# Kernel tuning notes

Hardware: AMD Instinct MI355X
Metric: run time of the kernel (lower is better)

## Reference

```python
import jax, jax.numpy as jnp
import numpy as np

H, HKV, HD = 16, 16, 64  # num_heads, num_kv_heads, head_dim

def rotate_half(x):
    x1, x2 = jnp.split(x, 2, axis=-1)
    return jnp.concatenate((-x2, x1), axis=-1)

def setup_inputs() -> dict:
    key = jax.random.key(0)
    ks = jax.random.split(key, 4)
    B, L, D = 4, 2048, 1024
    hidden_states = jax.random.normal(ks[0], (B, L, D), jnp.float32)
    # RoPE tables [L, head_dim]
    inv_freq = 1.0 / (10000.0 ** (jnp.arange(0, HD, 2, dtype=jnp.float32) / HD))
    freqs = jnp.outer(jnp.arange(L, dtype=jnp.float32), inv_freq)
    emb = jnp.concatenate((freqs, freqs), axis=-1)
    cos, sin = jnp.cos(emb), jnp.sin(emb)
    active_mask = jax.random.randint(ks[1], (B, L), 0, 2).astype(bool)
    Wqkv = jax.random.normal(ks[2], ((H + 2 * HKV) * HD, D), jnp.float32) / np.sqrt(D)
    Wo = jax.random.normal(ks[3], (D, H * HD), jnp.float32) / np.sqrt(H * HD)
    return {"hidden_states": hidden_states, "cos": cos, "sin": sin,
            "active_mask": active_mask, "Wqkv": Wqkv, "Wo": Wo}

def reference(hidden_states, cos, sin, active_mask, Wqkv, Wo):
    B, L, D = hidden_states.shape
    qkv = (hidden_states @ Wqkv.T).reshape(B, L, H + 2 * HKV, HD)
    q = qkv[:, :, :H]
    k = qkv[:, :, H:H + HKV]
    v = qkv[:, :, H + HKV:]
    c = cos[:, None, :]  # [L,1,HD] broadcasts over B and heads
    s = sin[:, None, :]
    q = q * c + rotate_half(q) * s
    k = k * c + rotate_half(k) * s
    # sparse queries: only active positions emit queries
    q = q * active_mask[:, :, None, None].astype(q.dtype)
    scale = 1.0 / np.sqrt(HD)
    scores = jnp.einsum('bqhd,bkhd->bhqk', q, k) * scale  # [B,H,L,L]
    attn = jax.nn.softmax(scores, axis=-1)
    out = jnp.einsum('bhqk,bkhd->bqhd', attn, v).reshape(B, L, H * HD)
    out = out @ Wo.T
    return out * active_mask[:, :, None].astype(out.dtype)
```

## Files before the change

### kernel.cpp

```cpp
#include <hip/hip_runtime.h>
#include <cstdint>

typedef _Float16 f16;
typedef __attribute__((ext_vector_type(2))) __fp16 fp16v2;
typedef __attribute__((ext_vector_type(4))) _Float16 f16x4;
typedef __attribute__((ext_vector_type(8))) _Float16 f16x8;
typedef __attribute__((ext_vector_type(4))) float f32x4;
typedef __attribute__((ext_vector_type(16))) float f32x16;

#if __has_builtin(__builtin_amdgcn_exp2f)
#define EXP2F(x) __builtin_amdgcn_exp2f(x)
#else
#define EXP2F(x) exp2f(x)
#endif

#if __has_builtin(__builtin_amdgcn_fdot2)
#define FDOT2(a, b, c) __builtin_amdgcn_fdot2((a), (b), (c), false)
#else
#define FDOT2(a, b, c) ((c) + (float)(a)[0] * (float)(b)[0] + (float)(a)[1] * (float)(b)[1])
#endif

#define GLOAD_LDS16(gp, lp) \
  __builtin_amdgcn_global_load_lds((const __attribute__((address_space(1))) void*)(gp), \
                                   (__attribute__((address_space(3))) void*)(lp), 16, 0, 0)

__global__ __launch_bounds__(256) void cvt_all(const float4* __restrict__ h, f16x4* __restrict__ h16,
                                               const float4* __restrict__ wq, f16x4* __restrict__ wq16,
                                               const float4* __restrict__ wo, f16x4* __restrict__ wo16,
                                               const float* __restrict__ cosb, const float* __restrict__ sinb,
                                               float2* __restrict__ cst) {
  int i = blockIdx.x * 256 + threadIdx.x;
  if (i >= 3145728) {
    const int i2 = i - 3145728;
    const int d = i2 >> 11, l = i2 & 2047;
    cst[i2] = make_float2(cosb[l * 64 + d], sinb[l * 64 + d]);
    return;
  }
  const float4* src;
  f16x4* dst;
  if (i < 2097152) { src = h + i; dst = h16 + i; }
  else if (i < 2883584) { src = wq + (i - 2097152); dst = wq16 + (i - 2097152); }
  else { src = wo + (i - 2883584); dst = wo16 + (i - 2883584); }
  float4 v = *src;
  f16x4 o;
  o.x = (f16)v.x; o.y = (f16)v.y; o.z = (f16)v.z; o.w = (f16)v.w;
  *dst = o;
}

template<int EPI, int N, int K>
__global__ __launch_bounds__(512) void gemm_bt2(
    const f16* __restrict__ A, const f16* __restrict__ Bm,
    f16* __restrict__ Qf, f16* __restrict__ Kf, f16* __restrict__ Vf,
    float* __restrict__ Cout, const int* __restrict__ mask,
    const float2* __restrict__ cst) {
  constexpr int NT = N / 128;
  constexpr int NKT = K / 64;
  const int tid = threadIdx.x;
  const int lane = tid & 63;
  const int wid = tid >> 6;
  const int wm = wid >> 1;
  const int wn = wid & 1;

  constexpr int nwg = 32 * NT;
  constexpr int cpx = nwg >> 3;
  const int swz = (blockIdx.x & 7) * cpx + (blockIdx.x >> 3);
  const int bm = swz / NT;
  const int bn = swz % NT;

  __shared__ f16 sA[2][256 * 64];
  __shared__ f16 sB[2][128 * 64];

  const f16* Abase = A + (size_t)bm * 256 * K;
  const f16* Bbase = Bm + (size_t)bn * 128 * K;

  f32x4 acc[4][4] = {};
  f16x8 af[4][2], bf[4][2];

  const int rowt = tid >> 3;
  const int c8 = (tid & 7) ^ (rowt & 7);
  const bool swp = (EPI == 1) && (bn < 16);

#define STAGE_KT(SLOT, KT)                                                      \
  do {                                                                          \
    _Pragma("unroll")                                                           \
    for (int g = 0; g < 4; ++g)                                                 \
      GLOAD_LDS16(Abase + (size_t)(g * 64 + rowt) * K + (KT) * 64 + c8 * 8,     \
                  &sA[SLOT][g * 4096 + tid * 8]);                               \
    _Pragma("unroll")                                                           \
    for (int g = 0; g < 2; ++g)                                                 \
      GLOAD_LDS16(Bbase + (size_t)(g * 64 + rowt) * K + (KT) * 64 + c8 * 8,     \
                  &sB[SLOT][g * 4096 + tid * 8]);                               \
  } while (0)

#define MFMA_CLUSTER(KS)                                                        \
  do {                                                                          \
    __builtin_amdgcn_s_setprio(1);                                              \
    if (swp) {                                                                  \
      _Pragma("unroll")                                                         \
      for (int i = 0; i < 4; ++i)                                               \
        _Pragma("unroll")                                                       \
        for (int j = 0; j < 4; ++j)                                             \
          acc[i][j] = __builtin_amdgcn_mfma_f32_16x16x32_f16(bf[i][KS], af[j][KS], acc[i][j], 0, 0, 0); \
    } else {                                                                    \
      _Pragma("unroll")                                                         \
      for (int i = 0; i < 4; ++i)                                               \
        _Pragma("unroll")                                                       \
        for (int j = 0; j < 4; ++j)                                             \
          acc[i][j] = __builtin_amdgcn_mfma_f32_16x16x32_f16(af[i][KS], bf[j][KS], acc[i][j], 0, 0, 0); \
    }                                                                           \
    __builtin_amdgcn_s_setprio(0);                                              \
  } while (0)

#define KTILE(VMC, DOSTAGE, KT, SLOT)                                           \
  do {                                                                          \
    asm volatile("s_waitcnt vmcnt(" #VMC ")" ::: "memory");                     \
    __builtin_amdgcn_s_barrier();                                               \
    __builtin_amdgcn_sched_barrier(0);                                          \
    _Pragma("unroll")                                                           \
    for (int i = 0; i < 4; ++i) {                                               \
      _Pragma("unroll")                                                         \
      for (int ks = 0; ks < 2; ++ks) {                                          \
        af[i][ks] = *(const f16x8*)&sA[SLOT][(wm * 64 + i * 16 + (lane & 15)) * 64 + ((ks * 4 + (lane >> 4)) ^ (lane & 7)) * 8]; \
        bf[i][ks] = *(const f16x8*)&sB[SLOT][(wn * 64 + i * 16 + (lane & 15)) * 64 + ((ks * 4 + (lane >> 4)) ^ (lane & 7)) * 8]; \
      }                                                                         \
    }                                                                           \
    MFMA_CLUSTER(0);                                                            \
    asm volatile("s_waitcnt lgkmcnt(0)" ::: "memory");                          \
    __builtin_amdgcn_sched_barrier(0);                                          \
    __builtin_amdgcn_s_barrier();                                               \
    if (DOSTAGE) { STAGE_KT(SLOT, (KT) + 2); }                                  \
    __builtin_amdgcn_sched_barrier(0);                                          \
    MFMA_CLUSTER(1);                                                            \
  } while (0)

  STAGE_KT(0, 0);
  STAGE_KT(1, 1);
#pragma unroll 1
  for (int it = 0; it < NKT - 2; it += 2) {
    KTILE(6, true, it, 0);
    KTILE(6, true, it + 1, 1);
  }
  KTILE(6, false, NKT - 2, 0);
  KTILE(0, false, NKT - 1, 1);

  const int lo = lane & 15;
  if constexpr (EPI == 1) {
    const int head = bn * 2 + wn;
    if (head < 32) {
      f16* dst = (head < 16) ? Qf : Kf;
      const int h15 = head & 15;
      const int h16l = lane >> 4;
      const int ahi = h16l >> 1, kkl = h16l & 1;
      #pragma unroll
      for (int j = 0; j < 4; ++j) {
        const int grow = bm * 256 + wm * 64 + j * 16 + lo;
        const int bb = grow >> 11, ll = grow & 2047;
        float msc = 1.0f;
        if (head < 16) msc = mask[bb * 2048 + ll] ? 0.18033688011112042f : 0.0f;
        f16* base = dst + (size_t)(bb * 16 + h15) * 64 * 2048;
        union { f16x8 v; fp16v2 hh[4]; } u0, u1;
        #pragma unroll
        for (int i = 0; i < 2; ++i) {
          float y0[4], y1[4];
          #pragma unroll
          for (int r = 0; r < 4; ++r) {
            const float2 cs = cst[(size_t)(i * 16 + 4 * h16l + r) * 2048 + ll];
            const float xl = acc[i][j][r], xh = acc[i + 2][j][r];
            y0[r] = (xl * cs.x - xh * cs.y) * msc;
            y1[r] = (xh * cs.x + xl * cs.y) * msc;
          }
          u0.hh[i * 2 + 0] = __builtin_amdgcn_cvt_pkrtz(y0[0], y0[1]);
          u0.hh[i * 2 + 1] = __builtin_amdgcn_cvt_pkrtz(y0[2], y0[3]);
          u1.hh[i * 2 + 0] = __builtin_amdgcn_cvt_pkrtz(y1[0], y1[1]);
          u1.hh[i * 2 + 1] = __builtin_amdgcn_cvt_pkrtz(y1[2], y1[3]);
        }
        const int t = ll >> 5, q5 = ll & 31;
        f16* p = base + (size_t)t * 2048 + (ahi * 32 + q5) * 8;
        *(f16x8*)(p + (kkl + 0) * 512) = u0.v;
        *(f16x8*)(p + (kkl + 2) * 512) = u1.v;
      }
    } else {
      const int hv = head - 32;
      #pragma unroll
      for (int i = 0; i < 4; ++i) {
        #pragma unroll
        for (int j = 0; j < 4; ++j) {
          #pragma unroll
          for (int r = 0; r < 4; ++r) {
            const int gm = bm * 256 + wm * 64 + i * 16 + (lane >> 4) * 4 + r;
            const int bb = gm >> 11, ll = gm & 2047;
            const int dd = j * 16 + lo;
            const int k = ll & 31;
            const int i32 = (k & ~12) | ((k & 4) << 1) | ((k & 8) >> 1);
            const int cc = i32 >> 4, hih = (i32 >> 3) & 1, jj = i32 & 7;
            const int blk = dd >> 5, qq = dd & 31;
            Vf[((size_t)(bb * 16 + hv) * 64 + (ll >> 5)) * 2048 +
               (cc * 2 + blk) * 512 + hih * 256 + qq * 8 + jj] = (f16)acc[i][j][r];
          }
        }
      }
    }
  } else {
    #pragma unroll
    for (int i = 0; i < 4; ++i) {
      #pragma unroll
      for (int j = 0; j < 4; ++j) {
        #pragma unroll
        for (int r = 0; r < 4; ++r) {
          const int gm = bm * 256 + wm * 64 + i * 16 + (lane >> 4) * 4 + r;
          const int gn = bn * 128 + wn * 64 + j * 16 + lo;
          const float mv = mask[gm] ? 1.0f : 0.0f;
          Cout[(size_t)gm * 1024 + gn] = acc[i][j][r] * mv;
        }
      }
    }
  }
#undef KTILE
#undef MFMA_CLUSTER
#undef STAGE_KT
}

#define LOADKV(kd, vd, kp, vp)                       \
  do {                                               \
    _Pragma("unroll")                                \
    for (int _i = 0; _i < 4; ++_i) {                 \
      kd[_i] = *(const f16x8*)&(kp)[_i * 512];       \
      vd[_i] = *(const f16x8*)&(vp)[_i * 512];       \
    }                                                \
  } while (0)

#define ATTN_BODY64(kr, vr)                                                      \
  do {                                                                           \
    f32x16 sa = {}, sb = {};                                                     \
    __builtin_amdgcn_s_setprio(1);                                               \
    _Pragma("unroll")                                                            \
    for (int _k = 0; _k < 4; ++_k)                                               \
      sa = __builtin_amdgcn_mfma_f32_32x32x16_f16(kr[_k], qfa[_k], sa, 0, 0, 0); \
    _Pragma("unroll")                                                            \
    for (int _k = 0; _k < 4; ++_k)                                               \
      sb = __builtin_amdgcn_mfma_f32_32x32x16_f16(kr[_k], qfb[_k], sb, 0, 0, 0); \
    __builtin_amdgcn_s_setprio(0);                                               \
    union PU { fp16v2 h[4]; f16x8 v; } pa0, pa1, pb0, pb1;                       \
    _Pragma("unroll")                                                            \
    for (int _i = 0; _i < 4; ++_i) {                                             \
      pa0.h[_i] = __builtin_amdgcn_cvt_pkrtz(EXP2F(sa[2 * _i]), EXP2F(sa[2 * _i + 1]));       \
      pa1.h[_i] = __builtin_amdgcn_cvt_pkrtz(EXP2F(sa[8 + 2 * _i]), EXP2F(sa[8 + 2 * _i + 1])); \
      la = FDOT2(pa0.h[_i], kOne, la);                                           \
      la = FDOT2(pa1.h[_i], kOne, la);                                           \
    }                                                                            \
    _Pragma("unroll")                                                            \
    for (int _i = 0; _i < 4; ++_i) {                                             \
      pb0.h[_i] = __builtin_amdgcn_cvt_pkrtz(EXP2F(sb[2 * _i]), EXP2F(sb[2 * _i + 1]));       \
      pb1.h[_i] = __builtin_amdgcn_cvt_pkrtz(EXP2F(sb[8 + 2 * _i]), EXP2F(sb[8 + 2 * _i + 1])); \
      lb = FDOT2(pb0.h[_i], kOne, lb);                                           \
      lb = FDOT2(pb1.h[_i], kOne, lb);                                           \
    }                                                                            \
    __builtin_amdgcn_s_setprio(1);                                               \
    oa0 = __builtin_amdgcn_mfma_f32_32x32x16_f16(vr[0], pa0.v, oa0, 0, 0, 0);    \
    oa1 = __builtin_amdgcn_mfma_f32_32x32x16_f16(vr[1], pa0.v, oa1, 0, 0, 0);    \
    ob0 = __builtin_amdgcn_mfma_f32_32x32x16_f16(vr[0], pb0.v, ob0, 0, 0, 0);    \
    ob1 = __builtin_amdgcn_mfma_f32_32x32x16_f16(vr[1], pb0.v, ob1, 0, 0, 0);    \
    oa0 = __builtin_amdgcn_mfma_f32_32x32x16_f16(vr[2], pa1.v, oa0, 0, 0, 0);    \
    oa1 = __builtin_amdgcn_mfma_f32_32x32x16_f16(vr[3], pa1.v, oa1, 0, 0, 0);    \
    ob0 = __builtin_amdgcn_mfma_f32_32x32x16_f16(vr[2], pb1.v, ob0, 0, 0, 0);    \
    ob1 = __builtin_amdgcn_mfma_f32_32x32x16_f16(vr[3], pb1.v, ob1, 0, 0, 0);    \
    __builtin_amdgcn_s_setprio(0);                                               \
  } while (0)

__global__ __launch_bounds__(512) void attn_kernel(const f16* __restrict__ Qf,
                                                   const f16* __restrict__ Kf,
                                                   const f16* __restrict__ Vf,
                                                   f16* __restrict__ Ow) {
  const int bid = (blockIdx.x & 7) * 64 + (blockIdx.x >> 3);
  const int bh = bid >> 3;
  const int qt = bid & 7;
  const int lane = threadIdx.x & 63;
  const int wid = threadIdx.x >> 6;
  const int qw = wid & 3;
  const int kvh = wid >> 2;
  const int hi = lane >> 5;
  const int q = lane & 31;

  __shared__ float o_lds[8][32][65];
  __shared__ float l_lds[8][32];

  const f16* Qb = Qf + (size_t)bh * 64 * 2048;
  const f16* Kb = Kf + (size_t)bh * 64 * 2048;
  const f16* Vb = Vf + (size_t)bh * 64 * 2048;

  const int ta = qt * 8 + qw * 2;
  f16x8 qfa[4], qfb[4];
  {
    const f16* pa = Qb + (size_t)ta * 2048 + lane * 8;
    const f16* pb = pa + 2048;
    #pragma unroll
    for (int kk = 0; kk < 4; ++kk) {
      qfa[kk] = *(const f16x8*)&pa[kk * 512];
      qfb[kk] = *(const f16x8*)&pb[kk * 512];
    }
  }

  f32x16 oa0 = {}, oa1 = {}, ob0 = {}, ob1 = {};
  float la = 0.0f, lb = 0.0f;
  const fp16v2 kOne = {(__fp16)1.0f, (__fp16)1.0f};

  const f16* kptr = Kb + (size_t)(kvh * 32) * 2048 + lane * 8;
  const f16* vptr = Vb + (size_t)(kvh * 32) * 2048 + lane * 8;
  f16x8 ka[4], va[4], kn[4], vn[4];
  LOADKV(ka, va, kptr, vptr);
  for (int t = 0; t < 32; t += 2) {
    LOADKV(kn, vn, kptr + 2048, vptr + 2048);
    ATTN_BODY64(ka, va);
    if (t + 2 < 32)
      LOADKV(ka, va, kptr + 4096, vptr + 4096);
    ATTN_BODY64(kn, vn);
    kptr += 4096; vptr += 4096;
  }

  float lha = la + __shfl_xor(la, 32, 64);
  float lhb = lb + __shfl_xor(lb, 32, 64);

  if (kvh == 1) {
    #pragma unroll
    for (int blk = 0; blk < 2; ++blk)
      #pragma unroll
      for (int g = 0; g < 4; ++g)
        #pragma unroll
        for (int j = 0; j < 4; ++j) {
          const int d = blk * 32 + g * 8 + 4 * hi + j;
          o_lds[qw * 2 + 0][q][d] = blk ? oa1[g * 4 + j] : oa0[g * 4 + j];
          o_lds[qw * 2 + 1][q][d] = blk ? ob1[g * 4 + j] : ob0[g * 4 + j];
        }
    if (hi == 0) { l_lds[qw * 2 + 0][q] = lha; l_lds[qw * 2 + 1][q] = lhb; }
  }
  __syncthreads();
  if (kvh == 0) {
    const float inva = 1.0f / (lha + l_lds[qw * 2 + 0][q]);
    const float invb = 1.0f / (lhb + l_lds[qw * 2 + 1][q]);
    const int b = bh >> 4, h = bh & 15;
    const int qra = qt * 256 + qw * 64 + q;
    f16* orowa = Ow + ((size_t)(b * 2048 + qra)) * 1024 + h * 64;
    f16* orowb = orowa + 32 * 1024;
    #pragma unroll
    for (int blk = 0; blk < 2; ++blk) {
      #pragma unroll
      for (int g = 0; g < 4; ++g) {
        f16x4 sta, stb;
        #pragma unroll
        for (int j = 0; j < 4; ++j) {
          const int d = blk * 32 + g * 8 + 4 * hi + j;
          sta[j] = (f16)(((blk ? oa1[g * 4 + j] : oa0[g * 4 + j]) + o_lds[qw * 2 + 0][q][d]) * inva);
          stb[j] = (f16)(((blk ? ob1[g * 4 + j] : ob0[g * 4 + j]) + o_lds[qw * 2 + 1][q][d]) * invb);
        }
        *(f16x4*)&orowa[blk * 32 + g * 8 + 4 * hi] = sta;
        *(f16x4*)&orowb[blk * 32 + g * 8 + 4 * hi] = stb;
      }
    }
  }
}

extern "C" void kernel_launch(void* const* d_in, const int* in_sizes, int n_in,
                              void* d_out, int out_size, void* d_ws, size_t ws_size,
                              hipStream_t stream) {
  const float* hidden = (const float*)d_in[0];
  const float* cosb   = (const float*)d_in[1];
  const float* sinb   = (const float*)d_in[2];
  const int*   mask   = (const int*)d_in[3];
  const float* wqkv   = (const float*)d_in[4];
  const float* wo     = (const float*)d_in[5];
  float* out = (float*)d_out;
  char* ws = (char*)d_ws;

  f16* h16    = (f16*)(ws + 0);
  f16* wqkv16 = (f16*)(ws + 16777216);
  f16* wo16   = (f16*)(ws + 23068672);
  f16* Qfb    = (f16*)(ws + 25165824);
  f16* Kfb    = (f16*)(ws + 41943040);
  f16* Vfb    = (f16*)(ws + 58720256);
  float2* cst = (float2*)(ws + 75497472);
  f16* Ow     = h16;

  cvt_all<<<12544, 256, 0, stream>>>((const float4*)hidden, (f16x4*)h16,
                                     (const float4*)wqkv, (f16x4*)wqkv16,
                                     (const float4*)wo, (f16x4*)wo16,
                                     cosb, sinb, cst);

  gemm_bt2<1, 3072, 1024><<<768, 512, 0, stream>>>(h16, wqkv16, Qfb, Kfb, Vfb,
                                                   nullptr, mask, cst);

  attn_kernel<<<512, 512, 0, stream>>>(Qfb, Kfb, Vfb, Ow);

  gemm_bt2<2, 1024, 1024><<<256, 512, 0, stream>>>(Ow, wo16, nullptr, nullptr, nullptr,
                                                   out, mask, nullptr);
}
```

Measured before the change: 162.8 us.

## Split attention KV range four ways per block with two-stage LDS reduction

Each attention block now handles 128 queries instead of 256, and its 8 waves split the key range into four slices instead of two. The launch doubles to 1024 blocks. Partial outputs are normalised, stored in LDS as f16, and merged in a two-level tree reduction weighted by the row sums. This raises parallelism and shortens each wave's serial KV loop. In exchange each block loads K/V twice as often overall, adds an extra barrier and reduction step, and loses some precision from storing the partials in f16.

```diff
diff --git a/kernel.cpp b/kernel.cpp
--- a/kernel.cpp
+++ b/kernel.cpp
@@ -271,24 +271,24 @@
                                                    const f16* __restrict__ Kf,
                                                    const f16* __restrict__ Vf,
                                                    f16* __restrict__ Ow) {
-  const int bid = (blockIdx.x & 7) * 64 + (blockIdx.x >> 3);
-  const int bh = bid >> 3;
-  const int qt = bid & 7;
+  const int bid = (blockIdx.x & 7) * 128 + (blockIdx.x >> 3);
+  const int bh = bid >> 4;
+  const int qt = bid & 15;
   const int lane = threadIdx.x & 63;
   const int wid = threadIdx.x >> 6;
-  const int qw = wid & 3;
-  const int kvh = wid >> 2;
+  const int qw = wid & 1;
+  const int kvs = wid >> 1;
   const int hi = lane >> 5;
   const int q = lane & 31;
 
-  __shared__ float o_lds[8][32][65];
-  __shared__ float l_lds[8][32];
+  __shared__ f16 o_lds[2][2][2][32][68];
+  __shared__ float l_lds[2][2][2][32];
 
   const f16* Qb = Qf + (size_t)bh * 64 * 2048;
   const f16* Kb = Kf + (size_t)bh * 64 * 2048;
   const f16* Vb = Vf + (size_t)bh * 64 * 2048;
 
-  const int ta = qt * 8 + qw * 2;
+  const int ta = qt * 4 + qw * 2;
   f16x8 qfa[4], qfb[4];
   {
     const f16* pa = Qb + (size_t)ta * 2048 + lane * 8;
@@ -304,14 +304,15 @@
   float la = 0.0f, lb = 0.0f;
   const fp16v2 kOne = {(__fp16)1.0f, (__fp16)1.0f};
 
-  const f16* kptr = Kb + (size_t)(kvh * 32) * 2048 + lane * 8;
-  const f16* vptr = Vb + (size_t)(kvh * 32) * 2048 + lane * 8;
+  const int tb = kvs * 16;
+  const f16* kptr = Kb + (size_t)tb * 2048 + lane * 8;
+  const f16* vptr = Vb + (size_t)tb * 2048 + lane * 8;
   f16x8 ka[4], va[4], kn[4], vn[4];
   LOADKV(ka, va, kptr, vptr);
-  for (int t = 0; t < 32; t += 2) {
+  for (int t = 0; t < 16; t += 2) {
     LOADKV(kn, vn, kptr + 2048, vptr + 2048);
     ATTN_BODY64(ka, va);
-    if (t + 2 < 32)
+    if (t + 2 < 16)
       LOADKV(ka, va, kptr + 4096, vptr + 4096);
     ATTN_BODY64(kn, vn);
     kptr += 4096; vptr += 4096;
@@ -320,37 +321,95 @@
   float lha = la + __shfl_xor(la, 32, 64);
   float lhb = lb + __shfl_xor(lb, 32, 64);
 
-  if (kvh == 1) {
+  if (kvs & 1) {
+    const int slot = kvs >> 1;
+    const float ia = 1.0f / lha, ib = 1.0f / lhb;
     #pragma unroll
     for (int blk = 0; blk < 2; ++blk)
       #pragma unroll
-      for (int g = 0; g < 4; ++g)
+      for (int g = 0; g < 4; ++g) {
+        f16x4 na, nb;
         #pragma unroll
         for (int j = 0; j < 4; ++j) {
-          const int d = blk * 32 + g * 8 + 4 * hi + j;
-          o_lds[qw * 2 + 0][q][d] = blk ? oa1[g * 4 + j] : oa0[g * 4 + j];
-          o_lds[qw * 2 + 1][q][d] = blk ? ob1[g * 4 + j] : ob0[g * 4 + j];
-        }
-    if (hi == 0) { l_lds[qw * 2 + 0][q] = lha; l_lds[qw * 2 + 1][q] = lhb; }
+          na[j] = (f16)((blk ? oa1[g * 4 + j] : oa0[g * 4 + j]) * ia);
+          nb[j] = (f16)((blk ? ob1[g * 4 + j] : ob0[g * 4 + j]) * ib);
+        }
+        const int d = blk * 32 + g * 8 + 4 * hi;
+        *(f16x4*)&o_lds[qw][slot][0][q][d] = na;
+        *(f16x4*)&o_lds[qw][slot][1][q][d] = nb;
+      }
+    if (hi == 0) { l_lds[qw][slot][0][q] = lha; l_lds[qw][slot][1][q] = lhb; }
   }
   __syncthreads();
-  if (kvh == 0) {
-    const float inva = 1.0f / (lha + l_lds[qw * 2 + 0][q]);
-    const float invb = 1.0f / (lhb + l_lds[qw * 2 + 1][q]);
+
+  float l01a = 0.0f, l01b = 0.0f;
+  if (!(kvs & 1)) {
+    const int slot = kvs >> 1;
+    const float lsa = l_lds[qw][slot][0][q];
+    const float lsb = l_lds[qw][slot][1][q];
+    l01a = lha + lsa;
+    l01b = lhb + lsb;
+    #pragma unroll
+    for (int blk = 0; blk < 2; ++blk)
+      #pragma unroll
+      for (int g = 0; g < 4; ++g) {
+        const int d = blk * 32 + g * 8 + 4 * hi;
+        const f16x4 na = *(const f16x4*)&o_lds[qw][slot][0][q][d];
+        const f16x4 nb = *(const f16x4*)&o_lds[qw][slot][1][q][d];
+        #pragma unroll
+        for (int j = 0; j < 4; ++j) {
+          if (blk) {
+            oa1[g * 4 + j] = oa1[g * 4 + j] + (float)na[j] * lsa;
+            ob1[g * 4 + j] = ob1[g * 4 + j] + (float)nb[j] * lsb;
+          } else {
+            oa0[g * 4 + j] = oa0[g * 4 + j] + (float)na[j] * lsa;
+            ob0[g * 4 + j] = ob0[g * 4 + j] + (float)nb[j] * lsb;
+          }
+        }
+      }
+    if (kvs == 2) {
+      const float ia = 1.0f / l01a, ib = 1.0f / l01b;
+      #pragma unroll
+      for (int blk = 0; blk < 2; ++blk)
+        #pragma unroll
+        for (int g = 0; g < 4; ++g) {
+          f16x4 na, nb;
+          #pragma unroll
+          for (int j = 0; j < 4; ++j) {
+            na[j] = (f16)((blk ? oa1[g * 4 + j] : oa0[g * 4 + j]) * ia);
+            nb[j] = (f16)((blk ? ob1[g * 4 + j] : ob0[g * 4 + j]) * ib);
+          }
+          const int d = blk * 32 + g * 8 + 4 * hi;
+          *(f16x4*)&o_lds[qw][1][0][q][d] = na;
+          *(f16x4*)&o_lds[qw][1][1][q][d] = nb;
+        }
+      if (hi == 0) { l_lds[qw][1][0][q] = l01a; l_lds[qw][1][1][q] = l01b; }
+    }
+  }
+  __syncthreads();
+
+  if (kvs == 0) {
+    const float l23a = l_lds[qw][1][0][q];
+    const float l23b = l_lds[qw][1][1][q];
+    const float inva = 1.0f / (l01a + l23a);
+    const float invb = 1.0f / (l01b + l23b);
+    const float wa = l23a * inva, wb = l23b * invb;
     const int b = bh >> 4, h = bh & 15;
-    const int qra = qt * 256 + qw * 64 + q;
+    const int qra = qt * 128 + qw * 64 + q;
     f16* orowa = Ow + ((size_t)(b * 2048 + qra)) * 1024 + h * 64;
     f16* orowb = orowa + 32 * 1024;
     #pragma unroll
     for (int blk = 0; blk < 2; ++blk) {
       #pragma unroll
       for (int g = 0; g < 4; ++g) {
+        const int d = blk * 32 + g * 8 + 4 * hi;
+        const f16x4 na = *(const f16x4*)&o_lds[qw][1][0][q][d];
+        const f16x4 nb = *(const f16x4*)&o_lds[qw][1][1][q][d];
         f16x4 sta, stb;
         #pragma unroll
         for (int j = 0; j < 4; ++j) {
-          const int d = blk * 32 + g * 8 + 4 * hi + j;
-          sta[j] = (f16)(((blk ? oa1[g * 4 + j] : oa0[g * 4 + j]) + o_lds[qw * 2 + 0][q][d]) * inva);
-          stb[j] = (f16)(((blk ? ob1[g * 4 + j] : ob0[g * 4 + j]) + o_lds[qw * 2 + 1][q][d]) * invb);
+          sta[j] = (f16)((blk ? oa1[g * 4 + j] : oa0[g * 4 + j]) * inva + (float)na[j] * wa);
+          stb[j] = (f16)((blk ? ob1[g * 4 + j] : ob0[g * 4 + j]) * invb + (float)nb[j] * wb);
         }
         *(f16x4*)&orowa[blk * 32 + g * 8 + 4 * hi] = sta;
         *(f16x4*)&orowb[blk * 32 + g * 8 + 4 * hi] = stb;
@@ -388,7 +447,7 @@
   gemm_bt2<1, 3072, 1024><<<768, 512, 0, stream>>>(h16, wqkv16, Qfb, Kfb, Vfb,
                                                    nullptr, mask, cst);
 
-  attn_kernel<<<512, 512, 0, stream>>>(Qfb, Kfb, Vfb, Ow);
+  attn_kernel<<<1024, 512, 0, stream>>>(Qfb, Kfb, Vfb, Ow);
 
   gemm_bt2<2, 1024, 1024><<<256, 512, 0, stream>>>(Ow, wo16, nullptr, nullptr, nullptr,
                                                    out, mask, nullptr);
```

New measurement: 168.6 us. 1.04x slower.

## Software-pipeline attention loop so QK MFMA of next tile overlaps softmax exp

Applied to the files above, without the earlier changes.

Splits the attention body into separate QK, exp/pack, and PV stages and reorders the loop so the next tile's QK^T MFMAs are issued while the current tile's exponentials are being computed. K and V loads are also decoupled and issued at different points. It interleaves the SA/SB MFMA chains and initialises them from a zero constant. The cost is an extra pair of score accumulators, which raises register pressure and may reduce occupancy.

```diff
diff --git a/kernel.cpp b/kernel.cpp
--- a/kernel.cpp
+++ b/kernel.cpp
@@ -220,41 +220,43 @@
 #undef STAGE_KT
 }
 
-#define LOADKV(kd, vd, kp, vp)                       \
+#define LOADK(kd, kp)                                \
   do {                                               \
     _Pragma("unroll")                                \
-    for (int _i = 0; _i < 4; ++_i) {                 \
+    for (int _i = 0; _i < 4; ++_i)                   \
       kd[_i] = *(const f16x8*)&(kp)[_i * 512];       \
-      vd[_i] = *(const f16x8*)&(vp)[_i * 512];       \
-    }                                                \
-  } while (0)
-
-#define ATTN_BODY64(kr, vr)                                                      \
+  } while (0)
+
+#define QKBODY(SA, SB, kr)                                                       \
   do {                                                                           \
-    f32x16 sa = {}, sb = {};                                                     \
     __builtin_amdgcn_s_setprio(1);                                               \
+    SA = __builtin_amdgcn_mfma_f32_32x32x16_f16(kr[0], qfa[0], z16, 0, 0, 0);    \
+    SB = __builtin_amdgcn_mfma_f32_32x32x16_f16(kr[0], qfb[0], z16, 0, 0, 0);    \
     _Pragma("unroll")                                                            \
-    for (int _k = 0; _k < 4; ++_k)                                               \
-      sa = __builtin_amdgcn_mfma_f32_32x32x16_f16(kr[_k], qfa[_k], sa, 0, 0, 0); \
-    _Pragma("unroll")                                                            \
-    for (int _k = 0; _k < 4; ++_k)                                               \
-      sb = __builtin_amdgcn_mfma_f32_32x32x16_f16(kr[_k], qfb[_k], sb, 0, 0, 0); \
+    for (int _k = 1; _k < 4; ++_k) {                                             \
+      SA = __builtin_amdgcn_mfma_f32_32x32x16_f16(kr[_k], qfa[_k], SA, 0, 0, 0); \
+      SB = __builtin_amdgcn_mfma_f32_32x32x16_f16(kr[_k], qfb[_k], SB, 0, 0, 0); \
+    }                                                                            \
     __builtin_amdgcn_s_setprio(0);                                               \
-    union PU { fp16v2 h[4]; f16x8 v; } pa0, pa1, pb0, pb1;                       \
+  } while (0)
+
+#define EXPPACK(SA, SB)                                                          \
+  do {                                                                           \
     _Pragma("unroll")                                                            \
     for (int _i = 0; _i < 4; ++_i) {                                             \
-      pa0.h[_i] = __builtin_amdgcn_cvt_pkrtz(EXP2F(sa[2 * _i]), EXP2F(sa[2 * _i + 1]));       \
-      pa1.h[_i] = __builtin_amdgcn_cvt_pkrtz(EXP2F(sa[8 + 2 * _i]), EXP2F(sa[8 + 2 * _i + 1])); \
+      pa0.h[_i] = __builtin_amdgcn_cvt_pkrtz(EXP2F(SA[2 * _i]), EXP2F(SA[2 * _i + 1]));       \
+      pa1.h[_i] = __builtin_amdgcn_cvt_pkrtz(EXP2F(SA[8 + 2 * _i]), EXP2F(SA[8 + 2 * _i + 1])); \
       la = FDOT2(pa0.h[_i], kOne, la);                                           \
       la = FDOT2(pa1.h[_i], kOne, la);                                           \
-    }                                                                            \
-    _Pragma("unroll")                                                            \
-    for (int _i = 0; _i < 4; ++_i) {                                             \
-      pb0.h[_i] = __builtin_amdgcn_cvt_pkrtz(EXP2F(sb[2 * _i]), EXP2F(sb[2 * _i + 1]));       \
-      pb1.h[_i] = __builtin_amdgcn_cvt_pkrtz(EXP2F(sb[8 + 2 * _i]), EXP2F(sb[8 + 2 * _i + 1])); \
+      pb0.h[_i] = __builtin_amdgcn_cvt_pkrtz(EXP2F(SB[2 * _i]), EXP2F(SB[2 * _i + 1]));       \
+      pb1.h[_i] = __builtin_amdgcn_cvt_pkrtz(EXP2F(SB[8 + 2 * _i]), EXP2F(SB[8 + 2 * _i + 1])); \
       lb = FDOT2(pb0.h[_i], kOne, lb);                                           \
       lb = FDOT2(pb1.h[_i], kOne, lb);                                           \
     }                                                                            \
+  } while (0)
+
+#define PVBODY(vr)                                                               \
+  do {                                                                           \
     __builtin_amdgcn_s_setprio(1);                                               \
     oa0 = __builtin_amdgcn_mfma_f32_32x32x16_f16(vr[0], pa0.v, oa0, 0, 0, 0);    \
     oa1 = __builtin_amdgcn_mfma_f32_32x32x16_f16(vr[1], pa0.v, oa1, 0, 0, 0);    \
@@ -301,21 +303,39 @@
   }
 
   f32x16 oa0 = {}, oa1 = {}, ob0 = {}, ob1 = {};
+  const f32x16 z16 = {};
   float la = 0.0f, lb = 0.0f;
   const fp16v2 kOne = {(__fp16)1.0f, (__fp16)1.0f};
-
-  const f16* kptr = Kb + (size_t)(kvh * 32) * 2048 + lane * 8;
-  const f16* vptr = Vb + (size_t)(kvh * 32) * 2048 + lane * 8;
-  f16x8 ka[4], va[4], kn[4], vn[4];
-  LOADKV(ka, va, kptr, vptr);
-  for (int t = 0; t < 32; t += 2) {
-    LOADKV(kn, vn, kptr + 2048, vptr + 2048);
-    ATTN_BODY64(ka, va);
-    if (t + 2 < 32)
-      LOADKV(ka, va, kptr + 4096, vptr + 4096);
-    ATTN_BODY64(kn, vn);
-    kptr += 4096; vptr += 4096;
-  }
+  union PU { fp16v2 h[4]; f16x8 v; } pa0, pa1, pb0, pb1;
+
+  const f16* kp = Kb + (size_t)(kvh * 32) * 2048 + lane * 8;
+  const f16* vp = Vb + (size_t)(kvh * 32) * 2048 + lane * 8;
+  f16x8 ka[4], kn[4], va[4], vn[4];
+  f32x16 sa, sb, sa2, sb2;
+
+  LOADK(ka, kp);  LOADK(va, vp);
+  LOADK(kn, kp + 2048);  LOADK(vn, vp + 2048);
+  QKBODY(sa, sb, ka);
+
+#pragma unroll 1
+  for (int t = 0; t < 30; t += 2) {
+    EXPPACK(sa, sb);
+    QKBODY(sa2, sb2, kn);
+    LOADK(ka, kp + 4096);
+    PVBODY(va);
+    LOADK(va, vp + 4096);
+    EXPPACK(sa2, sb2);
+    QKBODY(sa, sb, ka);
+    LOADK(kn, kp + 6144);
+    PVBODY(vn);
+    LOADK(vn, vp + 6144);
+    kp += 4096; vp += 4096;
+  }
+  EXPPACK(sa, sb);
+  QKBODY(sa2, sb2, kn);
+  PVBODY(va);
+  EXPPACK(sa2, sb2);
+  PVBODY(vn);
 
   float lha = la + __shfl_xor(la, 32, 64);
   float lhb = lb + __shfl_xor(lb, 32, 64);
```

Result: no change. 163.9 us (+0.7%).
